# Performance work log

Hardware: AMD Instinct MI355X
Metric: run time of the kernel (lower is better)

Reference implementation:

```python
import jax, jax.numpy as jnp
import numpy as np

N, E, F_IN, H, C = 50000, 800000, 128, 128, 64


def setup_inputs() -> dict:
    key = jax.random.key(0)
    ks = jax.random.split(key, 10)
    s = lambda f: np.float32(1.0 / np.sqrt(f))
    return {
        "x": jax.random.normal(ks[0], (N, F_IN), jnp.float32),
        "edge_index": jax.random.randint(ks[1], (2, E), 0, N, dtype=jnp.int64),
        # SAGEConv1: lin_l (on aggregated neighbors, with bias) + lin_r (on root, no bias)
        "W1l": jax.random.normal(ks[2], (F_IN, H), jnp.float32) * s(F_IN),
        "b1l": jnp.zeros((H,), jnp.float32),
        "W1r": jax.random.normal(ks[3], (F_IN, H), jnp.float32) * s(F_IN),
        # SAGEConv2
        "W2l": jax.random.normal(ks[4], (H, C), jnp.float32) * s(H),
        "b2l": jnp.zeros((C,), jnp.float32),
        "W2r": jax.random.normal(ks[5], (H, C), jnp.float32) * s(H),
        # GCNConv
        "Wg": jax.random.normal(ks[6], (C, C), jnp.float32) * s(C),
        "bg": jnp.zeros((C,), jnp.float32),
    }


def sage_conv(x, edge_index, Wl, bl, Wr):
    # PyG SAGEConv (mean aggr): out = lin_l(mean_{j in N(i)} x_j) + lin_r(x_i)
    n = x.shape[0]
    src, dst = edge_index[0], edge_index[1]
    agg = jax.ops.segment_sum(x[src], dst, num_segments=n)  # [N, F]
    cnt = jax.ops.segment_sum(jnp.ones((src.shape[0],), x.dtype), dst, num_segments=n)
    mean = agg / jnp.maximum(cnt, 1.0)[:, None]
    return mean @ Wl + bl + x @ Wr


def gcn_conv(x, edge_index, W, b):
    # PyG GCNConv: add self loops, symmetric normalization D^-1/2 A D^-1/2
    n = x.shape[0]
    loop = jnp.arange(n, dtype=edge_index.dtype)
    src = jnp.concatenate([edge_index[0], loop])
    dst = jnp.concatenate([edge_index[1], loop])
    deg = jax.ops.segment_sum(jnp.ones((src.shape[0],), x.dtype), dst, num_segments=n)
    dinv = jnp.where(deg > 0, jax.lax.rsqrt(jnp.maximum(deg, 1e-12)), 0.0)
    norm = dinv[src] * dinv[dst]  # [E+N]
    xw = x @ W
    out = jax.ops.segment_sum(xw[src] * norm[:, None], dst, num_segments=n)
    return out + b


def reference(x, edge_index, W1l, b1l, W1r, W2l, b2l, W2r, Wg, bg):
    h = jax.nn.relu(sage_conv(x, edge_index, W1l, b1l, W1r))
    # dropout is identity in eval mode
    h = sage_conv(h, edge_index, W2l, b2l, W2r)
    h = jax.nn.softmax(h, axis=1)  # activate='softmax'
    return gcn_conv(h, edge_index, Wg, bg)
```

## Files before the change

kernel.cpp:

```cpp
#include <hip/hip_runtime.h>
#include <hip/hip_fp16.h>
#include <math.h>


typedef __attribute__((ext_vector_type(8))) short bf16x8;
typedef __attribute__((ext_vector_type(4))) float f32x4;

__device__ inline unsigned short f32_bf16_hi(float f) {
    unsigned int u = __builtin_bit_cast(unsigned int, f);
    u = (u + 0x7FFFu + ((u >> 16) & 1u)) >> 16;
    return (unsigned short)u;
}
__device__ inline float bf16_to_f32(unsigned short h) {
    unsigned int u = ((unsigned int)h) << 16;
    return __builtin_bit_cast(float, u);
}

union H8 { float4 f4; __half2 h[4]; };

__global__ void count_kernel(const int* __restrict__ dst, int* __restrict__ off,
                             int E, int NB, int BK) {
    __shared__ int hist[256];
    int t = threadIdx.x;
    hist[t] = 0;
    __syncthreads();
    int base = blockIdx.x * 8192;
    for (int i = t; i < 8192; i += 256) {
        int e = base + i;
        if (e < E) atomicAdd(&hist[dst[e] >> 8], 1);
    }
    __syncthreads();
    if (t < BK) off[1 + t * NB + blockIdx.x] = hist[t];
    if (blockIdx.x == 0 && t == 0) off[0] = 0;
}

__global__ void scan_reduce_kernel(const int* __restrict__ data, int* __restrict__ bsum, int n) {
    __shared__ int red[256];
    int t = threadIdx.x;
    int base = blockIdx.x * 2048 + t * 8;
    int s = 0;
    if (base + 8 <= n) {
        int4 a = *(const int4*)(data + base);
        int4 b = *(const int4*)(data + base + 4);
        s = a.x + a.y + a.z + a.w + b.x + b.y + b.z + b.w;
    } else {
        for (int i = 0; i < 8; ++i)
            if (base + i < n) s += data[base + i];
    }
    red[t] = s;
    __syncthreads();
    for (int off = 128; off > 0; off >>= 1) {
        if (t < off) red[t] += red[t + off];
        __syncthreads();
    }
    if (t == 0) bsum[blockIdx.x] = red[0];
}

__global__ void scan_offsets_kernel(int* __restrict__ bsum, int B) {
    if (threadIdx.x == 0 && blockIdx.x == 0) {
        int run = 0;
        for (int i = 0; i < B; ++i) { int v = bsum[i]; bsum[i] = run; run += v; }
    }
}

__global__ void scan_final_kernel(int* __restrict__ data, const int* __restrict__ bsum, int n) {
    __shared__ int tsum[256];
    int t = threadIdx.x;
    int base = blockIdx.x * 2048 + t * 8;
    int v[8];
    int s = 0;
#pragma unroll
    for (int i = 0; i < 8; ++i) {
        v[i] = (base + i < n) ? data[base + i] : 0;
        s += v[i];
    }
    tsum[t] = s;
    for (int off = 1; off < 256; off <<= 1) {
        __syncthreads();
        int u = (t >= off) ? tsum[t - off] : 0;
        __syncthreads();
        tsum[t] += u;
    }
    __syncthreads();
    int run = bsum[blockIdx.x] + tsum[t] - s;
#pragma unroll
    for (int i = 0; i < 8; ++i) {
        run += v[i];
        if (base + i < n) data[base + i] = run;
    }
}

__global__ void partition_kernel(const int* __restrict__ src, const int* __restrict__ dst,
                                 const int* __restrict__ off, unsigned* __restrict__ ebuf,
                                 int E, int NB, int BK) {
    __shared__ int cur[256];
    int t = threadIdx.x;
    if (t < BK) cur[t] = off[t * NB + blockIdx.x];
    __syncthreads();
    int base = blockIdx.x * 8192;
    for (int i = t; i < 8192; i += 256) {
        int e = base + i;
        if (e < E) {
            int d = dst[e];
            int pos = atomicAdd(&cur[d >> 8], 1);
            ebuf[pos] = ((unsigned)src[e] << 8) | (unsigned)(d & 255);
        }
    }
}

__global__ void finalize_kernel(const unsigned* __restrict__ ebuf, const int* __restrict__ off,
                                int* __restrict__ col, int* __restrict__ rowptr,
                                float* __restrict__ dinv, int N, int NB, int E) {
    __shared__ int hist[256], scn[256], cur[256];
    int b = blockIdx.x, t = threadIdx.x;
    int base = off[b * NB];
    int end  = off[(b + 1) * NB];
    int M = end - base;
    hist[t] = 0;
    __syncthreads();
    for (int i = t; i < M; i += 256) atomicAdd(&hist[ebuf[base + i] & 255u], 1);
    __syncthreads();
    scn[t] = hist[t];
    for (int o = 1; o < 256; o <<= 1) {
        __syncthreads();
        int u = (t >= o) ? scn[t - o] : 0;
        __syncthreads();
        scn[t] += u;
    }
    __syncthreads();
    int excl = scn[t] - hist[t];
    int node = b * 256 + t;
    if (node < N) {
        rowptr[node] = base + excl;
        dinv[node] = rsqrtf((float)(hist[t] + 1));
    }
    if (b == 0 && t == 0) rowptr[N] = E;
    cur[t] = base + excl;
    __syncthreads();
    for (int i = t; i < M; i += 256) {
        unsigned w = ebuf[base + i];
        int pos = atomicAdd(&cur[w & 255u], 1);
        col[pos] = (int)(w >> 8);
    }
}

__global__ void packw_kernel(const float* __restrict__ W1l, const float* __restrict__ W1r,
                             const float* __restrict__ W2l, const float* __restrict__ W2r,
                             const float* __restrict__ Wg,
                             unsigned short* __restrict__ p1h, unsigned short* __restrict__ p1l,
                             unsigned short* __restrict__ p2h, unsigned short* __restrict__ p2l,
                             unsigned short* __restrict__ p3h, unsigned short* __restrict__ p3l) {
    int which = blockIdx.y;
    const float* W;
    unsigned short *hi, *lo;
    int K, Mp, colOff, T;
    if (which == 0)      { W = W1l; hi = p1h; lo = p1l; K = 128; Mp = 128; colOff = 0;   T = 16; }
    else if (which == 1) { W = W1r; hi = p1h; lo = p1l; K = 128; Mp = 128; colOff = 128; T = 16; }
    else if (which == 2) { W = W2l; hi = p2h; lo = p2l; K = 128; Mp = 64;  colOff = 0;   T = 8;  }
    else if (which == 3) { W = W2r; hi = p2h; lo = p2l; K = 128; Mp = 64;  colOff = 64;  T = 8;  }
    else                 { W = Wg;  hi = p3h; lo = p3l; K = 64;  Mp = 64;  colOff = 0;   T = 4;  }
    int idx = blockIdx.x * blockDim.x + threadIdx.x;
    if (idx >= K * Mp) return;
    int k = idx / Mp, m = idx % Mp;
    float w = W[(size_t)k * Mp + m];
    int colI = colOff + m;
    int s = k >> 5, kk = k & 31, qq = kk >> 3, j = kk & 7;
    int tt = colI >> 4, n = colI & 15;
    int lane = qq * 16 + n;
    size_t pos = ((size_t)(s * T + tt) * 64 + lane) * 8 + j;
    unsigned short h = f32_bf16_hi(w);
    hi[pos] = h;
    lo[pos] = f32_bf16_hi(w - bf16_to_f32(h));
}

__launch_bounds__(256)
__global__ void gemm1_kernel(const float* __restrict__ A,
                             const unsigned short* __restrict__ Whi,
                             const unsigned short* __restrict__ Wlo,
                             __half* __restrict__ outA, __half* __restrict__ outB, int N) {
    constexpr int Ttot = 16, TB = 8;
    const int lane = threadIdx.x & 63;
    const int wave = threadIdx.x >> 6;
    const int m = lane & 15, q = lane >> 4;
    const int t0 = blockIdx.y * TB;
    const int row0 = blockIdx.x * 64 + wave * 16;
    int arow = row0 + m;
    if (arow >= N) arow = N - 1;
    const float* ap = A + (size_t)arow * 128 + q * 8;

    float av[4][8];
#pragma unroll
    for (int s = 0; s < 4; ++s) {
        *(float4*)(av[s])     = *(const float4*)(ap + s * 32);
        *(float4*)(av[s] + 4) = *(const float4*)(ap + s * 32 + 4);
    }
    bf16x8 ahi[4], alo[4];
#pragma unroll
    for (int s = 0; s < 4; ++s)
#pragma unroll
        for (int i = 0; i < 8; ++i) {
            unsigned short h = f32_bf16_hi(av[s][i]);
            ahi[s][i] = (short)h;
            alo[s][i] = (short)f32_bf16_hi(av[s][i] - bf16_to_f32(h));
        }

    f32x4 acc[TB];
#pragma unroll
    for (int t = 0; t < TB; ++t) acc[t] = (f32x4)(0.f);
    const bf16x8* whp = (const bf16x8*)Whi;
    const bf16x8* wlp = (const bf16x8*)Wlo;
#pragma unroll
    for (int s = 0; s < 4; ++s) {
        const int base = (s * Ttot + t0) * 64 + lane;
#pragma unroll
        for (int t = 0; t < TB; ++t) {
            bf16x8 wh = whp[base + t * 64];
            bf16x8 wl = wlp[base + t * 64];
            acc[t] = __builtin_amdgcn_mfma_f32_16x16x32_bf16(ahi[s], wh, acc[t], 0, 0, 0);
            acc[t] = __builtin_amdgcn_mfma_f32_16x16x32_bf16(alo[s], wh, acc[t], 0, 0, 0);
            acc[t] = __builtin_amdgcn_mfma_f32_16x16x32_bf16(ahi[s], wl, acc[t], 0, 0, 0);
        }
    }

#pragma unroll
    for (int r = 0; r < 4; ++r) {
        int row = row0 + q * 4 + r;
        if (row < N) {
            __half* op = (blockIdx.y == 0) ? outA : outB;
#pragma unroll
            for (int t = 0; t < TB; ++t) {
                int c = (t0 + t) * 16 + m - blockIdx.y * 128;
                op[(size_t)row * 128 + c] = __float2half(acc[t][r]);
            }
        }
    }
}

__launch_bounds__(256)
__global__ void sage2_fused_kernel(const __half* __restrict__ p16, const __half* __restrict__ q16,
                                   const int* __restrict__ rowptr, const int* __restrict__ col,
                                   const float* __restrict__ b1l,
                                   const unsigned short* __restrict__ Whi,
                                   const unsigned short* __restrict__ Wlo,
                                   __half* __restrict__ r16, __half* __restrict__ s16, int N) {
    __shared__ float part[4][64][16];
    const int lane = threadIdx.x & 63;
    const int wave = threadIdx.x >> 6;
    const int pairH = wave & 1;
    const int grp   = wave >> 1;
    const int m = lane & 15, q = lane >> 4;
    const int row0 = blockIdx.x * 32 + grp * 16;
    int node = row0 + m;
    int nclamp = (node < N) ? node : (N - 1);
    int sAll = rowptr[nclamp];
    int eAll = (node < N) ? rowptr[nclamp + 1] : sAll;
    int deg  = eAll - sAll;
    int half0 = (deg + 1) >> 1;
    int sIdx = sAll + (pairH ? half0 : 0);
    int eIdx = pairH ? eAll : (sAll + half0);

    float acc[4][8];
#pragma unroll
    for (int s = 0; s < 4; ++s)
#pragma unroll
        for (int i = 0; i < 8; ++i) acc[s][i] = 0.f;

    const __half* pb = p16 + q * 8;
    int ptr = sIdx;
    for (; ptr + 4 <= eIdx; ptr += 4) {
        int j0 = col[ptr], j1 = col[ptr + 1], j2 = col[ptr + 2], j3 = col[ptr + 3];
        H8 u[4][4];
#pragma unroll
        for (int s = 0; s < 4; ++s) {
            u[0][s].f4 = *(const float4*)(pb + (size_t)j0 * 128 + s * 32);
            u[1][s].f4 = *(const float4*)(pb + (size_t)j1 * 128 + s * 32);
            u[2][s].f4 = *(const float4*)(pb + (size_t)j2 * 128 + s * 32);
            u[3][s].f4 = *(const float4*)(pb + (size_t)j3 * 128 + s * 32);
        }
#pragma unroll
        for (int s = 0; s < 4; ++s)
#pragma unroll
            for (int k = 0; k < 4; ++k) {
                float2 f0 = __half22float2(u[0][s].h[k]);
                float2 f1 = __half22float2(u[1][s].h[k]);
                float2 f2 = __half22float2(u[2][s].h[k]);
                float2 f3 = __half22float2(u[3][s].h[k]);
                acc[s][2 * k]     += (f0.x + f1.x) + (f2.x + f3.x);
                acc[s][2 * k + 1] += (f0.y + f1.y) + (f2.y + f3.y);
            }
    }
    for (; ptr < eIdx; ++ptr) {
        int j0 = col[ptr];
#pragma unroll
        for (int s = 0; s < 4; ++s) {
            H8 u0;
            u0.f4 = *(const float4*)(pb + (size_t)j0 * 128 + s * 32);
#pragma unroll
            for (int k = 0; k < 4; ++k) {
                float2 f0 = __half22float2(u0.h[k]);
                acc[s][2 * k]     += f0.x;
                acc[s][2 * k + 1] += f0.y;
            }
        }
    }

    float* ap = &acc[0][0];
    const int swz = lane & 3;
#pragma unroll
    for (int c = 0; c < 2; ++c) {
        if (c) __syncthreads();
#pragma unroll
        for (int sl = 0; sl < 4; ++sl)
            *(float4*)&part[wave][lane][(sl ^ swz) * 4] =
                *(const float4*)(ap + (c * 4 + sl) * 4);
        __syncthreads();
#pragma unroll
        for (int sl = 0; sl < 4; ++sl) {
            float4 pv = *(const float4*)&part[wave ^ 1][lane][(sl ^ swz) * 4];
            int g = (c * 4 + sl) * 4;
            ap[g]     += pv.x;
            ap[g + 1] += pv.y;
            ap[g + 2] += pv.z;
            ap[g + 3] += pv.w;
        }
    }

    float inv = 1.0f / fmaxf((float)deg, 1.0f);
    bf16x8 ahi[4], alo[4];
#pragma unroll
    for (int s = 0; s < 4; ++s) {
        H8 qv;
        qv.f4 = *(const float4*)(q16 + (size_t)nclamp * 128 + s * 32 + q * 8);
        float bv[8];
        *(float4*)(bv)     = *(const float4*)(b1l + s * 32 + q * 8);
        *(float4*)(bv + 4) = *(const float4*)(b1l + s * 32 + q * 8 + 4);
#pragma unroll
        for (int i = 0; i < 8; ++i) {
            float qf = __half2float(((const __half*)&qv)[i]);
            float h = fmaxf(acc[s][i] * inv + qf + bv[i], 0.f);
            unsigned short hb = f32_bf16_hi(h);
            ahi[s][i] = (short)hb;
            alo[s][i] = (short)f32_bf16_hi(h - bf16_to_f32(hb));
        }
    }

    f32x4 accm[4];
#pragma unroll
    for (int t = 0; t < 4; ++t) accm[t] = (f32x4)(0.f);
    const bf16x8* whp = (const bf16x8*)Whi;
    const bf16x8* wlp = (const bf16x8*)Wlo;
#pragma unroll
    for (int s = 0; s < 4; ++s) {
        const int base = (s * 8 + pairH * 4) * 64 + lane;
#pragma unroll
        for (int t = 0; t < 4; ++t) {
            bf16x8 wh = whp[base + t * 64];
            bf16x8 wl = wlp[base + t * 64];
            accm[t] = __builtin_amdgcn_mfma_f32_16x16x32_bf16(ahi[s], wh, accm[t], 0, 0, 0);
            accm[t] = __builtin_amdgcn_mfma_f32_16x16x32_bf16(alo[s], wh, accm[t], 0, 0, 0);
            accm[t] = __builtin_amdgcn_mfma_f32_16x16x32_bf16(ahi[s], wl, accm[t], 0, 0, 0);
        }
    }
    __half* op = pairH ? s16 : r16;
#pragma unroll
    for (int r = 0; r < 4; ++r) {
        int row = row0 + q * 4 + r;
        if (row < N) {
#pragma unroll
            for (int t = 0; t < 4; ++t) {
                int c = t * 16 + m;
                op[(size_t)row * 64 + c] = __float2half(accm[t][r]);
            }
        }
    }
}

__launch_bounds__(256)
__global__ void gcn_prep_fused_kernel(const __half* __restrict__ r16, const __half* __restrict__ s16,
                                      const int* __restrict__ rowptr, const int* __restrict__ col,
                                      const float* __restrict__ b2l,
                                      const unsigned short* __restrict__ Whi,
                                      const unsigned short* __restrict__ Wlo,
                                      const float* __restrict__ dinv,
                                      __half* __restrict__ tp16, int N) {
    __shared__ float part[4][64][16];
    const int lane = threadIdx.x & 63;
    const int wave = threadIdx.x >> 6;
    const int pairH = wave & 1;
    const int grp   = wave >> 1;
    const int m = lane & 15, q = lane >> 4;
    const int row0 = blockIdx.x * 32 + grp * 16;
    int node = row0 + m;
    int nclamp = (node < N) ? node : (N - 1);
    int sAll = rowptr[nclamp];
    int eAll = (node < N) ? rowptr[nclamp + 1] : sAll;
    int deg  = eAll - sAll;
    int half0 = (deg + 1) >> 1;
    int sIdx = sAll + (pairH ? half0 : 0);
    int eIdx = pairH ? eAll : (sAll + half0);

    float acc[2][8];
#pragma unroll
    for (int s = 0; s < 2; ++s)
#pragma unroll
        for (int i = 0; i < 8; ++i) acc[s][i] = 0.f;

    const __half* rb = r16 + q * 8;
    int ptr = sIdx;
    for (; ptr + 4 <= eIdx; ptr += 4) {
        int j0 = col[ptr], j1 = col[ptr + 1], j2 = col[ptr + 2], j3 = col[ptr + 3];
        H8 u[4][2];
#pragma unroll
        for (int s = 0; s < 2; ++s) {
            u[0][s].f4 = *(const float4*)(rb + (size_t)j0 * 64 + s * 32);
            u[1][s].f4 = *(const float4*)(rb + (size_t)j1 * 64 + s * 32);
            u[2][s].f4 = *(const float4*)(rb + (size_t)j2 * 64 + s * 32);
            u[3][s].f4 = *(const float4*)(rb + (size_t)j3 * 64 + s * 32);
        }
#pragma unroll
        for (int s = 0; s < 2; ++s)
#pragma unroll
            for (int k = 0; k < 4; ++k) {
                float2 f0 = __half22float2(u[0][s].h[k]);
                float2 f1 = __half22float2(u[1][s].h[k]);
                float2 f2 = __half22float2(u[2][s].h[k]);
                float2 f3 = __half22float2(u[3][s].h[k]);
                acc[s][2 * k]     += (f0.x + f1.x) + (f2.x + f3.x);
                acc[s][2 * k + 1] += (f0.y + f1.y) + (f2.y + f3.y);
            }
    }
    for (; ptr < eIdx; ++ptr) {
        int j0 = col[ptr];
#pragma unroll
        for (int s = 0; s < 2; ++s) {
            H8 u0;
            u0.f4 = *(const float4*)(rb + (size_t)j0 * 64 + s * 32);
#pragma unroll
            for (int k = 0; k < 4; ++k) {
                float2 f0 = __half22float2(u0.h[k]);
                acc[s][2 * k]     += f0.x;
                acc[s][2 * k + 1] += f0.y;
            }
        }
    }

    float* ap = &acc[0][0];
    const int swz = lane & 3;
#pragma unroll
    for (int sl = 0; sl < 4; ++sl)
        *(float4*)&part[wave][lane][(sl ^ swz) * 4] = *(const float4*)(ap + sl * 4);
    __syncthreads();
#pragma unroll
    for (int sl = 0; sl < 4; ++sl) {
        float4 pv = *(const float4*)&part[wave ^ 1][lane][(sl ^ swz) * 4];
        ap[sl * 4]     += pv.x;
        ap[sl * 4 + 1] += pv.y;
        ap[sl * 4 + 2] += pv.z;
        ap[sl * 4 + 3] += pv.w;
    }

    float inv = 1.0f / fmaxf((float)deg, 1.0f);
    float v[2][8];
    float mx = -1e30f;
#pragma unroll
    for (int s = 0; s < 2; ++s) {
        H8 sv;
        sv.f4 = *(const float4*)(s16 + (size_t)nclamp * 64 + s * 32 + q * 8);
        float bv[8];
        *(float4*)(bv)     = *(const float4*)(b2l + s * 32 + q * 8);
        *(float4*)(bv + 4) = *(const float4*)(b2l + s * 32 + q * 8 + 4);
#pragma unroll
        for (int i = 0; i < 8; ++i) {
            float sf = __half2float(((const __half*)&sv)[i]);
            v[s][i] = acc[s][i] * inv + sf + bv[i];
            mx = fmaxf(mx, v[s][i]);
        }
    }
    mx = fmaxf(mx, __shfl_xor(mx, 16, 64));
    mx = fmaxf(mx, __shfl_xor(mx, 32, 64));
    float sm = 0.f;
#pragma unroll
    for (int s = 0; s < 2; ++s)
#pragma unroll
        for (int i = 0; i < 8; ++i) {
            v[s][i] = expf(v[s][i] - mx);
            sm += v[s][i];
        }
    sm += __shfl_xor(sm, 16, 64);
    sm += __shfl_xor(sm, 32, 64);
    float is = 1.0f / sm;

    bf16x8 ahi[2], alo[2];
#pragma unroll
    for (int s = 0; s < 2; ++s)
#pragma unroll
        for (int i = 0; i < 8; ++i) {
            float h = v[s][i] * is;
            unsigned short hb = f32_bf16_hi(h);
            ahi[s][i] = (short)hb;
            alo[s][i] = (short)f32_bf16_hi(h - bf16_to_f32(hb));
        }

    f32x4 accm[2];
#pragma unroll
    for (int t = 0; t < 2; ++t) accm[t] = (f32x4)(0.f);
    const bf16x8* whp = (const bf16x8*)Whi;
    const bf16x8* wlp = (const bf16x8*)Wlo;
#pragma unroll
    for (int s = 0; s < 2; ++s) {
        const int base = (s * 4 + pairH * 2) * 64 + lane;
#pragma unroll
        for (int t = 0; t < 2; ++t) {
            bf16x8 wh = whp[base + t * 64];
            bf16x8 wl = wlp[base + t * 64];
            accm[t] = __builtin_amdgcn_mfma_f32_16x16x32_bf16(ahi[s], wh, accm[t], 0, 0, 0);
            accm[t] = __builtin_amdgcn_mfma_f32_16x16x32_bf16(alo[s], wh, accm[t], 0, 0, 0);
            accm[t] = __builtin_amdgcn_mfma_f32_16x16x32_bf16(ahi[s], wl, accm[t], 0, 0, 0);
        }
    }
#pragma unroll
    for (int r = 0; r < 4; ++r) {
        int row = row0 + q * 4 + r;
        if (row < N) {
            float sc = dinv[row];
#pragma unroll
            for (int t = 0; t < 2; ++t) {
                int c = (pairH * 2 + t) * 16 + m;
                tp16[(size_t)row * 64 + c] = __float2half(accm[t][r] * sc);
            }
        }
    }
}

__global__ void gcn_agg_kernel(const __half* __restrict__ tp,
                               const int* __restrict__ rowptr, const int* __restrict__ col,
                               const float* __restrict__ dinv, const float* __restrict__ bg,
                               float* __restrict__ out, int N) {
    int node = blockIdx.x * 4 + (threadIdx.x >> 6);
    if (node >= N) return;
    int lane = threadIdx.x & 63;
    int f2 = lane & 31;
    int ep = lane >> 5;
    int s = rowptr[node], e = rowptr[node + 1];
    float ax[8], ay[8];
#pragma unroll
    for (int k = 0; k < 8; ++k) { ax[k] = 0.f; ay[k] = 0.f; }
    int p = s;
    for (; p + 16 <= e; p += 16) {
#pragma unroll
        for (int k = 0; k < 8; ++k) {
            int j = col[p + 2 * k + ep];
            float2 f = __half22float2(*(const __half2*)(tp + (size_t)j * 64 + 2 * f2));
            ax[k] += f.x;
            ay[k] += f.y;
        }
    }
    for (int t = p + ep; t < e; t += 2) {
        int j = col[t];
        float2 f = __half22float2(*(const __half2*)(tp + (size_t)j * 64 + 2 * f2));
        ax[0] += f.x;
        ay[0] += f.y;
    }
    float sx = ((ax[0] + ax[1]) + (ax[2] + ax[3])) + ((ax[4] + ax[5]) + (ax[6] + ax[7]));
    float sy = ((ay[0] + ay[1]) + (ay[2] + ay[3])) + ((ay[4] + ay[5]) + (ay[6] + ay[7]));
    sx += __shfl_xor(sx, 32, 64);
    sy += __shfl_xor(sy, 32, 64);
    if (ep == 0) {
        float2 selfv = __half22float2(*(const __half2*)(tp + (size_t)node * 64 + 2 * f2));
        float di = dinv[node];
        float2 o;
        o.x = (sx + selfv.x) * di + bg[2 * f2];
        o.y = (sy + selfv.y) * di + bg[2 * f2 + 1];
        *(float2*)(out + (size_t)node * 64 + 2 * f2) = o;
    }
}

extern "C" void kernel_launch(void* const* d_in, const int* in_sizes, int n_in,
                              void* d_out, int out_size, void* d_ws, size_t ws_size,
                              hipStream_t stream) {
    const float* x = (const float*)d_in[0];
    const int* ei = (const int*)d_in[1];
    const float* W1l = (const float*)d_in[2];
    const float* b1l = (const float*)d_in[3];
    const float* W1r = (const float*)d_in[4];
    const float* W2l = (const float*)d_in[5];
    const float* b2l = (const float*)d_in[6];
    const float* W2r = (const float*)d_in[7];
    const float* Wg  = (const float*)d_in[8];
    const float* bg  = (const float*)d_in[9];

    const int N = in_sizes[0] / 128;
    const int E = in_sizes[1] / 2;
    const int* srcp = ei;
    const int* dstp = ei + E;

    const int NB = (E + 8191) / 8192;
    const int BK = (N + 255) >> 8;
    const int len = BK * NB;

    float* ws = (float*)d_ws;
    float* dinv = ws;
    __half* p16 = (__half*)(dinv + N);
    __half* q16 = p16 + (size_t)N * 128;
    __half* r16 = q16 + (size_t)N * 128;
    __half* s16 = r16 + (size_t)N * 64;
    __half* tp16 = s16 + (size_t)N * 64;
    int* rowptr = (int*)(tp16 + (size_t)N * 64);
    int* off    = rowptr + (N + 1);
    int* colbuf = off + len + 2;
    unsigned* ebuf = (unsigned*)(colbuf + E);
    int* bsum   = (int*)(ebuf + E);
    uintptr_t up = (uintptr_t)(bsum + 32);
    up = (up + 15) & ~(uintptr_t)15;
    unsigned short* p1h = (unsigned short*)up;
    unsigned short* p1l = p1h + 32768;
    unsigned short* p2h = p1l + 32768;
    unsigned short* p2l = p2h + 16384;
    unsigned short* p3h = p2l + 16384;
    unsigned short* p3l = p3h + 4096;

    float* out = (float*)d_out;

    count_kernel<<<NB, 256, 0, stream>>>(dstp, off, E, NB, BK);
    const int sn = len + 1;
    const int SBs = (sn + 2047) / 2048;
    scan_reduce_kernel<<<SBs, 256, 0, stream>>>(off, bsum, sn);
    scan_offsets_kernel<<<1, 64, 0, stream>>>(bsum, SBs);
    scan_final_kernel<<<SBs, 256, 0, stream>>>(off, bsum, sn);
    partition_kernel<<<NB, 256, 0, stream>>>(srcp, dstp, off, ebuf, E, NB, BK);
    finalize_kernel<<<BK, 256, 0, stream>>>(ebuf, off, colbuf, rowptr, dinv, N, NB, E);

    packw_kernel<<<dim3(64, 5), 256, 0, stream>>>(W1l, W1r, W2l, W2r, Wg,
                                                  p1h, p1l, p2h, p2l, p3h, p3l);

    const int gb  = (N + 63) / 64;
    const int gbf = (N + 31) / 32;
    const int ab  = (N + 3) / 4;

    gemm1_kernel<<<dim3(gb, 2), 256, 0, stream>>>(x, p1h, p1l, p16, q16, N);

    sage2_fused_kernel<<<gbf, 256, 0, stream>>>(p16, q16, rowptr, colbuf, b1l,
                                                p2h, p2l, r16, s16, N);

    gcn_prep_fused_kernel<<<gbf, 256, 0, stream>>>(r16, s16, rowptr, colbuf, b2l,
                                                   p3h, p3l, dinv, tp16, N);

    gcn_agg_kernel<<<ab, 256, 0, stream>>>(tp16, rowptr, colbuf, dinv, bg, out, N);
}
```

Before: 282.6 us.

## Store gathered layer-1 neighbor projection in FP8 to halve gather traffic

The projected neighbor features (x@W1l) that the sage2 kernel gathers per edge are now written as FP8 (e4m3) instead of FP16. gemm1 packs them through a swizzled shared-memory tile so each row goes out with coalesced 16-byte stores, and sage2 loads 8 bytes per lane and converts with packed fp8->f32 instructions. The aim is to halve the bytes moved in the dominant random-gather stage, at the cost of a large precision loss that may break accuracy tolerances.

```diff
diff --git a/kernel.cpp b/kernel.cpp
--- a/kernel.cpp
+++ b/kernel.cpp
@@ -5,6 +5,7 @@
 
 typedef __attribute__((ext_vector_type(8))) short bf16x8;
 typedef __attribute__((ext_vector_type(4))) float f32x4;
+typedef __attribute__((ext_vector_type(2))) float f32v2;
 
 __device__ inline unsigned short f32_bf16_hi(float f) {
     unsigned int u = __builtin_bit_cast(unsigned int, f);
@@ -177,8 +178,9 @@
 __global__ void gemm1_kernel(const float* __restrict__ A,
                              const unsigned short* __restrict__ Whi,
                              const unsigned short* __restrict__ Wlo,
-                             __half* __restrict__ outA, __half* __restrict__ outB, int N) {
+                             unsigned char* __restrict__ outA8, __half* __restrict__ outB, int N) {
     constexpr int Ttot = 16, TB = 8;
+    __shared__ __align__(16) unsigned char pk[4][16][128];
     const int lane = threadIdx.x & 63;
     const int wave = threadIdx.x >> 6;
     const int m = lane & 15, q = lane >> 4;
@@ -222,22 +224,45 @@
         }
     }
 
-#pragma unroll
-    for (int r = 0; r < 4; ++r) {
-        int row = row0 + q * 4 + r;
-        if (row < N) {
-            __half* op = (blockIdx.y == 0) ? outA : outB;
-#pragma unroll
-            for (int t = 0; t < TB; ++t) {
-                int c = (t0 + t) * 16 + m - blockIdx.y * 128;
-                op[(size_t)row * 128 + c] = __float2half(acc[t][r]);
+    if (blockIdx.y == 0) {
+#pragma unroll
+        for (int r = 0; r < 4; ++r) {
+            int row = q * 4 + r;
+            int sw = (row & 3) << 5;
+#pragma unroll
+            for (int t = 0; t < 8; t += 2) {
+                int w = __builtin_amdgcn_cvt_pk_fp8_f32(acc[t][r], acc[t + 1][r], 0, false);
+                pk[wave][row][(t * 16 + m) ^ sw] = (unsigned char)(w & 0xff);
+                pk[wave][row][((t + 1) * 16 + m) ^ sw] = (unsigned char)((w >> 8) & 0xff);
             }
         }
+        __syncthreads();
+        int rr = lane >> 2, qt = lane & 3;
+        int grow = row0 + rr;
+        if (grow < N) {
+            const unsigned char* srcp = &pk[wave][rr][(qt ^ (rr & 3)) * 32];
+            uint4 v0 = *(const uint4*)(srcp);
+            uint4 v1 = *(const uint4*)(srcp + 16);
+            *(uint4*)(outA8 + (size_t)grow * 128 + qt * 32) = v0;
+            *(uint4*)(outA8 + (size_t)grow * 128 + qt * 32 + 16) = v1;
+        }
+    } else {
+#pragma unroll
+        for (int r = 0; r < 4; ++r) {
+            int row = row0 + q * 4 + r;
+            if (row < N) {
+#pragma unroll
+                for (int t = 0; t < TB; ++t) {
+                    int c = (t0 + t) * 16 + m - 128;
+                    outB[(size_t)row * 128 + c] = __float2half(acc[t][r]);
+                }
+            }
+        }
     }
 }
 
 __launch_bounds__(256)
-__global__ void sage2_fused_kernel(const __half* __restrict__ p16, const __half* __restrict__ q16,
+__global__ void sage2_fused_kernel(const unsigned char* __restrict__ p8, const __half* __restrict__ q16,
                                    const int* __restrict__ rowptr, const int* __restrict__ col,
                                    const float* __restrict__ b1l,
                                    const unsigned short* __restrict__ Whi,
@@ -265,42 +290,45 @@
 #pragma unroll
         for (int i = 0; i < 8; ++i) acc[s][i] = 0.f;
 
-    const __half* pb = p16 + q * 8;
+    const unsigned char* pb = p8 + q * 8;
     int ptr = sIdx;
     for (; ptr + 4 <= eIdx; ptr += 4) {
         int j0 = col[ptr], j1 = col[ptr + 1], j2 = col[ptr + 2], j3 = col[ptr + 3];
-        H8 u[4][4];
+        uint2 u[4][4];
 #pragma unroll
         for (int s = 0; s < 4; ++s) {
-            u[0][s].f4 = *(const float4*)(pb + (size_t)j0 * 128 + s * 32);
-            u[1][s].f4 = *(const float4*)(pb + (size_t)j1 * 128 + s * 32);
-            u[2][s].f4 = *(const float4*)(pb + (size_t)j2 * 128 + s * 32);
-            u[3][s].f4 = *(const float4*)(pb + (size_t)j3 * 128 + s * 32);
+            u[0][s] = *(const uint2*)(pb + (size_t)j0 * 128 + s * 32);
+            u[1][s] = *(const uint2*)(pb + (size_t)j1 * 128 + s * 32);
+            u[2][s] = *(const uint2*)(pb + (size_t)j2 * 128 + s * 32);
+            u[3][s] = *(const uint2*)(pb + (size_t)j3 * 128 + s * 32);
         }
 #pragma unroll
         for (int s = 0; s < 4; ++s)
 #pragma unroll
-            for (int k = 0; k < 4; ++k) {
-                float2 f0 = __half22float2(u[0][s].h[k]);
-                float2 f1 = __half22float2(u[1][s].h[k]);
-                float2 f2 = __half22float2(u[2][s].h[k]);
-                float2 f3 = __half22float2(u[3][s].h[k]);
-                acc[s][2 * k]     += (f0.x + f1.x) + (f2.x + f3.x);
-                acc[s][2 * k + 1] += (f0.y + f1.y) + (f2.y + f3.y);
+            for (int e = 0; e < 4; ++e) {
+                f32v2 a = __builtin_amdgcn_cvt_pk_f32_fp8(u[e][s].x, false);
+                f32v2 b = __builtin_amdgcn_cvt_pk_f32_fp8(u[e][s].x, true);
+                f32v2 c = __builtin_amdgcn_cvt_pk_f32_fp8(u[e][s].y, false);
+                f32v2 d = __builtin_amdgcn_cvt_pk_f32_fp8(u[e][s].y, true);
+                acc[s][0] += a[0]; acc[s][1] += a[1];
+                acc[s][2] += b[0]; acc[s][3] += b[1];
+                acc[s][4] += c[0]; acc[s][5] += c[1];
+                acc[s][6] += d[0]; acc[s][7] += d[1];
             }
     }
     for (; ptr < eIdx; ++ptr) {
         int j0 = col[ptr];
 #pragma unroll
         for (int s = 0; s < 4; ++s) {
-            H8 u0;
-            u0.f4 = *(const float4*)(pb + (size_t)j0 * 128 + s * 32);
-#pragma unroll
-            for (int k = 0; k < 4; ++k) {
-                float2 f0 = __half22float2(u0.h[k]);
-                acc[s][2 * k]     += f0.x;
-                acc[s][2 * k + 1] += f0.y;
-            }
+            uint2 u0 = *(const uint2*)(pb + (size_t)j0 * 128 + s * 32);
+            f32v2 a = __builtin_amdgcn_cvt_pk_f32_fp8(u0.x, false);
+            f32v2 b = __builtin_amdgcn_cvt_pk_f32_fp8(u0.x, true);
+            f32v2 c = __builtin_amdgcn_cvt_pk_f32_fp8(u0.y, false);
+            f32v2 d = __builtin_amdgcn_cvt_pk_f32_fp8(u0.y, true);
+            acc[s][0] += a[0]; acc[s][1] += a[1];
+            acc[s][2] += b[0]; acc[s][3] += b[1];
+            acc[s][4] += c[0]; acc[s][5] += c[1];
+            acc[s][6] += d[0]; acc[s][7] += d[1];
         }
     }
 
@@ -600,8 +628,8 @@
 
     float* ws = (float*)d_ws;
     float* dinv = ws;
-    __half* p16 = (__half*)(dinv + N);
-    __half* q16 = p16 + (size_t)N * 128;
+    unsigned char* p8 = (unsigned char*)(dinv + N);
+    __half* q16 = (__half*)(p8 + (size_t)N * 128);
     __half* r16 = q16 + (size_t)N * 128;
     __half* s16 = r16 + (size_t)N * 64;
     __half* tp16 = s16 + (size_t)N * 64;
@@ -637,9 +665,9 @@
     const int gbf = (N + 31) / 32;
     const int ab  = (N + 3) / 4;
 
-    gemm1_kernel<<<dim3(gb, 2), 256, 0, stream>>>(x, p1h, p1l, p16, q16, N);
-
-    sage2_fused_kernel<<<gbf, 256, 0, stream>>>(p16, q16, rowptr, colbuf, b1l,
+    gemm1_kernel<<<dim3(gb, 2), 256, 0, stream>>>(x, p1h, p1l, p8, q16, N);
+
+    sage2_fused_kernel<<<gbf, 256, 0, stream>>>(p8, q16, rowptr, colbuf, b1l,
                                                 p2h, p2l, r16, s16, N);
 
     gcn_prep_fused_kernel<<<gbf, 256, 0, stream>>>(r16, s16, rowptr, colbuf, b2l,
```

Result: faster. 269.7 us (-4.5%).
